# Optimization experiments

Hardware: AMD Instinct MI355X
Metric: run time of the kernel (lower is better)

The kernel has to match this reference:

```python
import jax, jax.numpy as jnp
import numpy as np

GAM1 = 1.0
GAM2 = 1.0
EPS = 0.01


def setup_inputs() -> dict:
    key = jax.random.key(0)
    kx, ky = jax.random.split(key)
    m, p, k = 16384, 512, 10
    X = jax.random.normal(kx, (m, p), dtype=jnp.float32)
    Y = jax.random.randint(ky, (m,), 0, k, dtype=jnp.int64)
    return {"X": X, "Y": Y, "num_classes": k}


def reference(X, Y, num_classes):
    # W: [p, m] (features x samples), as in the torch module (W = X.T)
    W = X.reshape(X.shape[0], -1).T
    p, m = W.shape
    I = jnp.eye(p, dtype=W.dtype)

    # ---- empirical discriminative loss ----
    scalar = p / (m * EPS)
    G = W @ W.T  # [p, p]
    discrimn = jnp.linalg.slogdet(I + GAM1 * scalar * G)[1] / 2.0

    # ---- empirical compressive loss ----
    # Pi[j] is diagonal with the one-hot membership of class j, so
    # W @ Pi[j] @ W.T == (W * mask_j) @ W.T. Build all k masked Grams at once.
    M = jax.nn.one_hot(Y, num_classes, dtype=W.dtype)  # [m, k]
    trPi = M.sum(axis=0) + 1e-8                         # [k] class counts
    # Gk[j] = sum_{i in class j} w_i w_i^T  -> [k, p, p]
    Gk = jnp.einsum('pm,mk,qm->kpq', W, M, W)
    scal = (p / (trPi * EPS))[:, None, None]
    logdets = jnp.linalg.slogdet(I[None] + scal * Gk)[1]  # [k]
    compress = jnp.sum(logdets * trPi / m) / 2.0

    return (discrimn, compress)
```

## Files before the change

kernel.cpp:

```cpp
#include <hip/hip_runtime.h>
#include <math.h>

#define P 512
#define KC 10
#define NB 32
#define EPSV 0.01f
#define TR_ROWS 448
#define XT 17024

typedef __attribute__((ext_vector_type(8))) __bf16 bf16x8;
typedef __attribute__((ext_vector_type(4))) float floatx4;

__global__ __launch_bounds__(256) void sort_k(const int* __restrict__ Y, int* __restrict__ colmap,
                                              int* __restrict__ counts, int* __restrict__ off_pad, int m){
  __shared__ int cnt[KC], offp[KC + 1], cur[KC];
  int tid = threadIdx.x;
  if (tid < KC) cnt[tid] = 0;
  __syncthreads();
  for (int i = tid; i < m; i += 256){
    int y = Y[i];
    if (y >= 0 && y < KC) atomicAdd(&cnt[y], 1);
  }
  __syncthreads();
  if (tid == 0){
    int s = 0;
    for (int j = 0; j < KC; ++j){ offp[j] = s; s += ((cnt[j] + 63) >> 6) << 6; }
    offp[KC] = s;
  }
  __syncthreads();
  if (tid < KC){ cur[tid] = offp[tid]; counts[tid] = cnt[tid]; off_pad[tid] = offp[tid]; }
  if (tid == KC) off_pad[KC] = offp[KC];
  for (int i = tid; i < XT; i += 256) colmap[i] = -1;
  __syncthreads();
  for (int i = tid; i < m; i += 256){
    int y = Y[i];
    if (y >= 0 && y < KC){
      int pos = atomicAdd(&cur[y], 1);
      colmap[pos] = i;
    }
  }
}

__global__ __launch_bounds__(256) void xt_k(const float* __restrict__ X, const int* __restrict__ colmap,
                                            __bf16* __restrict__ Xhi, __bf16* __restrict__ Xlo){
  __shared__ float T[64][65];
  int c0 = blockIdx.x * 64;
  int f0 = blockIdx.y * 64;
  int tid = threadIdx.x;

  int j = tid >> 2;
  int piece = tid & 3;
  int s = colmap[c0 + j];
  if (s >= 0){
    const float* src = X + (long)s * P + f0 + piece * 16;
    #pragma unroll
    for (int q = 0; q < 4; ++q){
      float4 v = *(const float4*)(src + q * 4);
      T[piece * 16 + q * 4 + 0][j] = v.x;
      T[piece * 16 + q * 4 + 1][j] = v.y;
      T[piece * 16 + q * 4 + 2][j] = v.z;
      T[piece * 16 + q * 4 + 3][j] = v.w;
    }
  } else {
    #pragma unroll
    for (int q = 0; q < 16; ++q) T[piece * 16 + q][j] = 0.f;
  }
  __syncthreads();

  int f = tid >> 2;
  int cp = (tid & 3) * 16;
  bf16x8 vh0, vl0, vh1, vl1;
  #pragma unroll
  for (int q = 0; q < 8; ++q){
    float x0 = T[f][cp + q];
    float x1 = T[f][cp + 8 + q];
    __bf16 h0 = (__bf16)x0, h1 = (__bf16)x1;
    vh0[q] = h0; vl0[q] = (__bf16)(x0 - (float)h0);
    vh1[q] = h1; vl1[q] = (__bf16)(x1 - (float)h1);
  }
  long base = (long)(f0 + f) * XT + c0 + cp;
  *(bf16x8*)&Xhi[base]     = vh0;
  *(bf16x8*)&Xhi[base + 8] = vh1;
  *(bf16x8*)&Xlo[base]     = vl0;
  *(bf16x8*)&Xlo[base + 8] = vl1;
}

__global__ __launch_bounds__(256) void gram_mfma(const __bf16* __restrict__ Xhi,
                                                 const __bf16* __restrict__ Xlo,
                                                 const int* __restrict__ counts,
                                                 const int* __restrict__ off_pad,
                                                 float* __restrict__ Gk){
  int cls = blockIdx.y;
  int ta = 0, rem = blockIdx.x;
  while (rem >= ta + 1){ rem -= ta + 1; ++ta; }
  int tb = rem;
  int a0 = ta * 64, b0 = tb * 64;

  int tid  = threadIdx.x;
  int lane = tid & 63;
  int wv   = tid >> 6;
  int wrow = wv >> 1, wcol = wv & 1;
  int fr   = lane & 15;
  int quad = lane >> 4;

  int cs0     = off_pad[cls];
  int nchunks = (counts[cls] + 31) >> 5;

  long arow0 = (long)(a0 + wrow * 32 + fr) * XT;
  long brow0 = (long)(b0 + wcol * 32 + fr) * XT;

  floatx4 acc[2][2];
  #pragma unroll
  for (int i = 0; i < 2; ++i)
    #pragma unroll
    for (int j = 0; j < 2; ++j) acc[i][j] = (floatx4){0.f, 0.f, 0.f, 0.f};

  for (int ch = 0; ch < nchunks; ++ch){
    long co = cs0 + ch * 32 + quad * 8;
    bf16x8 ah[2], al[2], bh[2], bl[2];
    #pragma unroll
    for (int r = 0; r < 2; ++r){
      ah[r] = *(const bf16x8*)&Xhi[arow0 + (long)r * 16 * XT + co];
      al[r] = *(const bf16x8*)&Xlo[arow0 + (long)r * 16 * XT + co];
      bh[r] = *(const bf16x8*)&Xhi[brow0 + (long)r * 16 * XT + co];
      bl[r] = *(const bf16x8*)&Xlo[brow0 + (long)r * 16 * XT + co];
    }
    #pragma unroll
    for (int ri = 0; ri < 2; ++ri)
      #pragma unroll
      for (int rj = 0; rj < 2; ++rj){
        acc[ri][rj] = __builtin_amdgcn_mfma_f32_16x16x32_bf16(al[ri], bh[rj], acc[ri][rj], 0, 0, 0);
        acc[ri][rj] = __builtin_amdgcn_mfma_f32_16x16x32_bf16(ah[ri], bl[rj], acc[ri][rj], 0, 0, 0);
        acc[ri][rj] = __builtin_amdgcn_mfma_f32_16x16x32_bf16(ah[ri], bh[rj], acc[ri][rj], 0, 0, 0);
      }
  }

  float* C = Gk + (long)cls * P * P;
  #pragma unroll
  for (int ri = 0; ri < 2; ++ri){
    int a = a0 + wrow * 32 + ri * 16 + (lane >> 4) * 4;
    #pragma unroll
    for (int rj = 0; rj < 2; ++rj){
      int b = b0 + wcol * 32 + rj * 16 + (lane & 15);
      #pragma unroll
      for (int r = 0; r < 4; ++r)
        C[(long)(a + r) * P + b] = acc[ri][rj][r];
    }
  }
}

__global__ __launch_bounds__(256) void sum10_k(float* __restrict__ Gk){
  long i = (long)blockIdx.x * 256 + threadIdx.x;
  float4 s = {0.f, 0.f, 0.f, 0.f};
  #pragma unroll
  for (int j = 0; j < KC; ++j){
    float4 v = ((const float4*)(Gk + (long)j * P * P))[i];
    s.x += v.x; s.y += v.y; s.z += v.z; s.w += v.w;
  }
  ((float4*)(Gk + (long)KC * P * P))[i] = s;
}

__global__ __launch_bounds__(512, 2) void chol_mfma(float* __restrict__ Gk,
                                                    const int* __restrict__ counts,
                                                    float* __restrict__ logdets,
                                                    float m_tot){
  __shared__ __bf16 Lhi[TR_ROWS * 32];
  __shared__ __bf16 Llo[TR_ROWS * 32];
  __shared__ float  Ld[NB * 33];
  __shared__ float  Ldr[NB];

  int mat  = blockIdx.x;
  int tid  = threadIdx.x;
  int lane = tid & 63;
  int wv   = tid >> 6;
  float* A = Gk + (long)mat * P * P;
  float sc = (mat < KC) ? ((float)P / (((float)counts[mat] + 1e-8f) * EPSV))
                        : ((float)P / (m_tot * EPSV));
  float logsum = 0.f;

  for (int s = 0; s < 16; ++s){
    int j0 = s * NB;
    int qt = P - j0 - NB;

    if (wv == 0){
      float a[NB];
      if (lane < NB){
        const float* src = A + (long)(j0 + lane) * P + j0;
        #pragma unroll
        for (int u = 0; u < NB; u += 4){
          float4 v = *(const float4*)(src + u);
          a[u] = v.x; a[u+1] = v.y; a[u+2] = v.z; a[u+3] = v.w;
        }
        if (s == 0){
          #pragma unroll
          for (int u = 0; u < NB; ++u) a[u] *= sc;
          a[lane] += 1.0f;
        }
      } else {
        #pragma unroll
        for (int u = 0; u < NB; ++u) a[u] = 0.f;
      }
      #pragma unroll
      for (int jj = 0; jj < NB; ++jj){
        float d = __shfl(a[jj], jj);
        logsum += __log2f(d);
        float inv = 1.0f / d;
        float rs  = rsqrtf(d);
        float w   = a[jj] * inv;
        #pragma unroll
        for (int l = 0; l < NB; ++l){
          if (l > jj){
            float prl = __shfl(a[l], jj);
            a[l] -= w * prl;
          }
        }
        a[jj] *= rs;
      }
      if (lane < NB){
        #pragma unroll
        for (int u = 0; u < NB; ++u) Ld[lane * 33 + u] = a[u];
        Ldr[lane] = 1.0f / a[lane];
      }
    }
    __syncthreads();

    if (qt > 0){
      if (tid < qt){
        float b[NB];
        const float* src = A + (long)(j0 + NB + tid) * P + j0;
        #pragma unroll
        for (int u = 0; u < NB; u += 4){
          float4 v = *(const float4*)(src + u);
          b[u] = v.x; b[u+1] = v.y; b[u+2] = v.z; b[u+3] = v.w;
        }
        if (s == 0){
          #pragma unroll
          for (int u = 0; u < NB; ++u) b[u] *= sc;
        }
        #pragma unroll
        for (int jj = 0; jj < NB; ++jj){
          float acc = b[jj];
          for (int u = 0; u < jj; ++u) acc -= b[u] * Ld[jj * 33 + u];
          b[jj] = acc * Ldr[jj];
        }
        int t = tid;
        #pragma unroll
        for (int c = 0; c < 4; ++c){
          int sw = (t * 4 + (c ^ ((t >> 1) & 3))) * 8;
          bf16x8 vh, vl;
          #pragma unroll
          for (int j = 0; j < 8; ++j){
            float f = b[c * 8 + j];
            __bf16 h = (__bf16)f;
            vh[j] = h;
            vl[j] = (__bf16)(f - (float)h);
          }
          *(bf16x8*)&Lhi[sw] = vh;
          *(bf16x8*)&Llo[sw] = vl;
        }
      }
    }
    __syncthreads();

    if (qt > 0){
      int tt = qt >> 5;
      int T  = tt * (tt + 1) / 2;
      int trail0 = j0 + NB;
      for (int idx = wv; idx < T; idx += 8){
        int ti = 0, rem = idx;
        while (rem >= ti + 1){ rem -= ti + 1; ++ti; }
        int tj = rem;
        int I0 = ti * 32, J0 = tj * 32;
        int c  = lane >> 4;

        bf16x8 ahi[2], alo[2], bhi[2], blo[2];
        #pragma unroll
        for (int h = 0; h < 2; ++h){
          int r1 = I0 + h * 16 + (lane & 15);
          int sw1 = (r1 * 4 + (c ^ ((r1 >> 1) & 3))) * 8;
          ahi[h] = *(const bf16x8*)&Lhi[sw1];
          alo[h] = *(const bf16x8*)&Llo[sw1];
          int r2 = J0 + h * 16 + (lane & 15);
          int sw2 = (r2 * 4 + (c ^ ((r2 >> 1) & 3))) * 8;
          bhi[h] = *(const bf16x8*)&Lhi[sw2];
          blo[h] = *(const bf16x8*)&Llo[sw2];
        }

        #pragma unroll
        for (int hi_ = 0; hi_ < 2; ++hi_){
          #pragma unroll
          for (int hj = 0; hj < 2; ++hj){
            floatx4 acc = {0.f, 0.f, 0.f, 0.f};
            acc = __builtin_amdgcn_mfma_f32_16x16x32_bf16(alo[hi_], bhi[hj], acc, 0, 0, 0);
            acc = __builtin_amdgcn_mfma_f32_16x16x32_bf16(ahi[hi_], blo[hj], acc, 0, 0, 0);
            acc = __builtin_amdgcn_mfma_f32_16x16x32_bf16(ahi[hi_], bhi[hj], acc, 0, 0, 0);
            int grow0 = trail0 + I0 + hi_ * 16 + (lane >> 4) * 4;
            int gcol  = trail0 + J0 + hj  * 16 + (lane & 15);
            #pragma unroll
            for (int r = 0; r < 4; ++r){
              long off = (long)(grow0 + r) * P + gcol;
              float v = A[off];
              if (s == 0) v = sc * v + ((grow0 + r) == gcol ? 1.f : 0.f);
              A[off] = v - acc[r];
            }
          }
        }
      }
    }
    __syncthreads();
  }

  if (tid == 0) logdets[mat] = logsum * 0.6931471805599453f;
}

__global__ __launch_bounds__(64) void final_k(const float* __restrict__ logdets,
                                              const int* __restrict__ counts,
                                              float* __restrict__ out, float m_tot){
  if (threadIdx.x == 0 && blockIdx.x == 0){
    out[0] = 0.5f * logdets[KC];
    float comp = 0.f;
    for (int j = 0; j < KC; ++j){
      float trPi = (float)counts[j] + 1e-8f;
      comp += logdets[j] * trPi / m_tot;
    }
    out[1] = 0.5f * comp;
  }
}

extern "C" void kernel_launch(void* const* d_in, const int* in_sizes, int n_in,
                              void* d_out, int out_size, void* d_ws, size_t ws_size,
                              hipStream_t stream) {
  (void)n_in; (void)out_size; (void)ws_size;
  const float* X = (const float*)d_in[0];
  const int*   Y = (const int*)d_in[1];
  int m = in_sizes[0] / P;

  float*  Gk      = (float*)d_ws;
  __bf16* Xhi     = (__bf16*)(Gk + 11L * P * P);
  __bf16* Xlo     = Xhi + (long)P * XT;
  int*    colmap  = (int*)(Xlo + (long)P * XT);
  int*    counts  = colmap + XT;
  int*    off_pad = counts + 16;
  float*  logdets = (float*)(off_pad + 17);

  sort_k<<<1, 256, 0, stream>>>(Y, colmap, counts, off_pad, m);

  dim3 xg(XT / 64, 8);
  xt_k<<<xg, 256, 0, stream>>>(X, colmap, Xhi, Xlo);

  dim3 gg(36, KC);
  gram_mfma<<<gg, 256, 0, stream>>>(Xhi, Xlo, counts, off_pad, Gk);

  sum10_k<<<P * P / 1024, 256, 0, stream>>>(Gk);

  chol_mfma<<<KC + 1, 512, 0, stream>>>(Gk, counts, logdets, (float)m);

  final_k<<<1, 64, 0, stream>>>(logdets, counts, (float*)d_out, (float)m);
}
```

Measured before the change: 457.4 us.

## Replace panel triangular solve with explicit L^-1 and split-bf16 MFMA multiply

The diagonal-block wave now explicitly inverts the 32x32 Cholesky factor via readlane-based forward substitution and stores it as hi/lo bf16 in shared memory. The panel TRSM, previously a serial per-thread 32x32 triangular solve run by only qt threads, becomes a 3-pass split-bf16 MFMA product of each 16-row tile with L^-1, spread over all waves. Shuffles in the factorization are replaced with readlane. This moves serial scalar work onto matrix cores and raises parallelism in the panel step. In exchange it adds an explicit inversion and the accuracy risk of bf16-split arithmetic with an inverted factor.

```diff
diff --git a/kernel.cpp b/kernel.cpp
--- a/kernel.cpp
+++ b/kernel.cpp
@@ -7,9 +7,14 @@
 #define EPSV 0.01f
 #define TR_ROWS 448
 #define XT 17024
+#define MSTRIDE 40
 
 typedef __attribute__((ext_vector_type(8))) __bf16 bf16x8;
 typedef __attribute__((ext_vector_type(4))) float floatx4;
+
+__device__ __forceinline__ float rdl(float x, int l){
+  return __builtin_bit_cast(float, __builtin_amdgcn_readlane(__builtin_bit_cast(int, x), l));
+}
 
 __global__ __launch_bounds__(256) void sort_k(const int* __restrict__ Y, int* __restrict__ colmap,
                                               int* __restrict__ counts, int* __restrict__ off_pad, int m){
@@ -164,10 +169,10 @@
                                                     const int* __restrict__ counts,
                                                     float* __restrict__ logdets,
                                                     float m_tot){
-  __shared__ __bf16 Lhi[TR_ROWS * 32];
-  __shared__ __bf16 Llo[TR_ROWS * 32];
-  __shared__ float  Ld[NB * 33];
-  __shared__ float  Ldr[NB];
+  __shared__ __align__(16) __bf16 Lhi[TR_ROWS * 32];
+  __shared__ __align__(16) __bf16 Llo[TR_ROWS * 32];
+  __shared__ __align__(16) __bf16 Mhi[NB * MSTRIDE];
+  __shared__ __align__(16) __bf16 Mlo[NB * MSTRIDE];
 
   int mat  = blockIdx.x;
   int tid  = threadIdx.x;
@@ -184,6 +189,7 @@
 
     if (wv == 0){
       float a[NB];
+      float dri[NB];
       if (lane < NB){
         const float* src = A + (long)(j0 + lane) * P + j0;
         #pragma unroll
@@ -202,61 +208,84 @@
       }
       #pragma unroll
       for (int jj = 0; jj < NB; ++jj){
-        float d = __shfl(a[jj], jj);
+        float d = rdl(a[jj], jj);
         logsum += __log2f(d);
         float inv = 1.0f / d;
         float rs  = rsqrtf(d);
-        float w   = a[jj] * inv;
-        #pragma unroll
-        for (int l = 0; l < NB; ++l){
-          if (l > jj){
-            float prl = __shfl(a[l], jj);
-            a[l] -= w * prl;
-          }
+        dri[jj] = rs;
+        float w = a[jj] * inv;
+        #pragma unroll
+        for (int l = jj + 1; l < NB; ++l){
+          float prl = rdl(a[l], jj);
+          a[l] = fmaf(-w, prl, a[l]);
         }
         a[jj] *= rs;
       }
+      float mcol[NB];
+      #pragma unroll
+      for (int u = 0; u < NB; ++u) mcol[u] = 0.f;
+      #pragma unroll
+      for (int r = 0; r < NB; ++r){
+        float ssum = (lane == r) ? 1.0f : 0.0f;
+        #pragma unroll
+        for (int u = 0; u < r; ++u){
+          float lru = rdl(a[u], r);
+          ssum = fmaf(-lru, mcol[u], ssum);
+        }
+        mcol[r] = ssum * dri[r];
+      }
       if (lane < NB){
         #pragma unroll
-        for (int u = 0; u < NB; ++u) Ld[lane * 33 + u] = a[u];
-        Ldr[lane] = 1.0f / a[lane];
+        for (int u = 0; u < NB; ++u){
+          float f = mcol[u];
+          __bf16 h = (__bf16)f;
+          Mhi[u * MSTRIDE + lane] = h;
+          Mlo[u * MSTRIDE + lane] = (__bf16)(f - (float)h);
+        }
       }
     }
     __syncthreads();
 
     if (qt > 0){
-      if (tid < qt){
-        float b[NB];
-        const float* src = A + (long)(j0 + NB + tid) * P + j0;
-        #pragma unroll
-        for (int u = 0; u < NB; u += 4){
-          float4 v = *(const float4*)(src + u);
-          b[u] = v.x; b[u+1] = v.y; b[u+2] = v.z; b[u+3] = v.w;
-        }
+      int ntiles = qt >> 4;
+      int r16 = lane & 15;
+      int kq  = lane >> 4;
+      for (int rt = wv; rt < ntiles; rt += 8){
+        int row = j0 + NB + rt * 16 + r16;
+        const float* src = A + (long)row * P + j0 + kq * 8;
+        float4 v0 = *(const float4*)(src);
+        float4 v1 = *(const float4*)(src + 4);
+        float f[8] = {v0.x, v0.y, v0.z, v0.w, v1.x, v1.y, v1.z, v1.w};
         if (s == 0){
           #pragma unroll
-          for (int u = 0; u < NB; ++u) b[u] *= sc;
-        }
-        #pragma unroll
-        for (int jj = 0; jj < NB; ++jj){
-          float acc = b[jj];
-          for (int u = 0; u < jj; ++u) acc -= b[u] * Ld[jj * 33 + u];
-          b[jj] = acc * Ldr[jj];
-        }
-        int t = tid;
-        #pragma unroll
-        for (int c = 0; c < 4; ++c){
-          int sw = (t * 4 + (c ^ ((t >> 1) & 3))) * 8;
-          bf16x8 vh, vl;
+          for (int u = 0; u < 8; ++u) f[u] *= sc;
+        }
+        bf16x8 ahi, alo;
+        #pragma unroll
+        for (int u = 0; u < 8; ++u){
+          __bf16 h = (__bf16)f[u];
+          ahi[u] = h;
+          alo[u] = (__bf16)(f[u] - (float)h);
+        }
+        #pragma unroll
+        for (int ng = 0; ng < 2; ++ng){
+          int mrow = ng * 16 + r16;
+          bf16x8 bhi = *(const bf16x8*)&Mhi[mrow * MSTRIDE + kq * 8];
+          bf16x8 blo = *(const bf16x8*)&Mlo[mrow * MSTRIDE + kq * 8];
+          floatx4 acc = {0.f, 0.f, 0.f, 0.f};
+          acc = __builtin_amdgcn_mfma_f32_16x16x32_bf16(alo, bhi, acc, 0, 0, 0);
+          acc = __builtin_amdgcn_mfma_f32_16x16x32_bf16(ahi, blo, acc, 0, 0, 0);
+          acc = __builtin_amdgcn_mfma_f32_16x16x32_bf16(ahi, bhi, acc, 0, 0, 0);
           #pragma unroll
-          for (int j = 0; j < 8; ++j){
-            float f = b[c * 8 + j];
-            __bf16 h = (__bf16)f;
-            vh[j] = h;
-            vl[j] = (__bf16)(f - (float)h);
+          for (int r = 0; r < 4; ++r){
+            int t  = rt * 16 + kq * 4 + r;
+            int cc = ng * 16 + r16;
+            int e  = (t * 4 + ((cc >> 3) ^ ((t >> 1) & 3))) * 8 + (cc & 7);
+            float fv = acc[r];
+            __bf16 h = (__bf16)fv;
+            Lhi[e] = h;
+            Llo[e] = (__bf16)(fv - (float)h);
           }
-          *(bf16x8*)&Lhi[sw] = vh;
-          *(bf16x8*)&Llo[sw] = vl;
         }
       }
     }
@@ -273,17 +302,17 @@
         int I0 = ti * 32, J0 = tj * 32;
         int c  = lane >> 4;
 
-        bf16x8 ahi[2], alo[2], bhi[2], blo[2];
+        bf16x8 ahi2[2], alo2[2], bhi2[2], blo2[2];
         #pragma unroll
         for (int h = 0; h < 2; ++h){
           int r1 = I0 + h * 16 + (lane & 15);
           int sw1 = (r1 * 4 + (c ^ ((r1 >> 1) & 3))) * 8;
-          ahi[h] = *(const bf16x8*)&Lhi[sw1];
-          alo[h] = *(const bf16x8*)&Llo[sw1];
+          ahi2[h] = *(const bf16x8*)&Lhi[sw1];
+          alo2[h] = *(const bf16x8*)&Llo[sw1];
           int r2 = J0 + h * 16 + (lane & 15);
           int sw2 = (r2 * 4 + (c ^ ((r2 >> 1) & 3))) * 8;
-          bhi[h] = *(const bf16x8*)&Lhi[sw2];
-          blo[h] = *(const bf16x8*)&Llo[sw2];
+          bhi2[h] = *(const bf16x8*)&Lhi[sw2];
+          blo2[h] = *(const bf16x8*)&Llo[sw2];
         }
 
         #pragma unroll
@@ -291,9 +320,9 @@
           #pragma unroll
           for (int hj = 0; hj < 2; ++hj){
             floatx4 acc = {0.f, 0.f, 0.f, 0.f};
-            acc = __builtin_amdgcn_mfma_f32_16x16x32_bf16(alo[hi_], bhi[hj], acc, 0, 0, 0);
-            acc = __builtin_amdgcn_mfma_f32_16x16x32_bf16(ahi[hi_], blo[hj], acc, 0, 0, 0);
-            acc = __builtin_amdgcn_mfma_f32_16x16x32_bf16(ahi[hi_], bhi[hj], acc, 0, 0, 0);
+            acc = __builtin_amdgcn_mfma_f32_16x16x32_bf16(alo2[hi_], bhi2[hj], acc, 0, 0, 0);
+            acc = __builtin_amdgcn_mfma_f32_16x16x32_bf16(ahi2[hi_], blo2[hj], acc, 0, 0, 0);
+            acc = __builtin_amdgcn_mfma_f32_16x16x32_bf16(ahi2[hi_], bhi2[hj], acc, 0, 0, 0);
             int grow0 = trail0 + I0 + hi_ * 16 + (lane >> 4) * 4;
             int gcol  = trail0 + J0 + hj  * 16 + (lane & 15);
             #pragma unroll
```

Measured after the change: 503.3 us. 1.1x slower.

## Split-K the class Gram kernel with atomic accumulation and register prefetch

Applied to the files above, without the earlier changes.

Splits each class's sample-chunk reduction across four blocks along a new grid z dimension. Partial tiles are accumulated into Gk with atomicAdd after a memset zeroes the buffer. This raises the grid from 360 to 1440 blocks to fill more CUs. The inner loop also double-buffers the global loads so the next chunk is fetched while the current MFMAs run. The cost is atomic traffic, an extra memset, and non-deterministic float summation order.

```diff
diff --git a/kernel.cpp b/kernel.cpp
--- a/kernel.cpp
+++ b/kernel.cpp
@@ -7,6 +7,7 @@
 #define EPSV 0.01f
 #define TR_ROWS 448
 #define XT 17024
+#define KSPLIT 4
 
 typedef __attribute__((ext_vector_type(8))) __bf16 bf16x8;
 typedef __attribute__((ext_vector_type(4))) float floatx4;
@@ -105,6 +106,9 @@
 
   int cs0     = off_pad[cls];
   int nchunks = (counts[cls] + 31) >> 5;
+  int nper    = (nchunks + KSPLIT - 1) / KSPLIT;
+  int ch0     = blockIdx.z * nper;
+  int ch1     = min(nchunks, ch0 + nper);
 
   long arow0 = (long)(a0 + wrow * 32 + fr) * XT;
   long brow0 = (long)(b0 + wcol * 32 + fr) * XT;
@@ -115,25 +119,35 @@
     #pragma unroll
     for (int j = 0; j < 2; ++j) acc[i][j] = (floatx4){0.f, 0.f, 0.f, 0.f};
 
-  for (int ch = 0; ch < nchunks; ++ch){
-    long co = cs0 + ch * 32 + quad * 8;
+#define GLOAD(AH, AL, BH, BL, CH)                                            \
+  { long co = cs0 + (long)(CH) * 32 + quad * 8;                              \
+    for (int r = 0; r < 2; ++r){                                             \
+      AH[r] = *(const bf16x8*)&Xhi[arow0 + (long)r * 16 * XT + co];          \
+      AL[r] = *(const bf16x8*)&Xlo[arow0 + (long)r * 16 * XT + co];          \
+      BH[r] = *(const bf16x8*)&Xhi[brow0 + (long)r * 16 * XT + co];          \
+      BL[r] = *(const bf16x8*)&Xlo[brow0 + (long)r * 16 * XT + co]; } }
+
+  if (ch0 < ch1){
     bf16x8 ah[2], al[2], bh[2], bl[2];
-    #pragma unroll
-    for (int r = 0; r < 2; ++r){
-      ah[r] = *(const bf16x8*)&Xhi[arow0 + (long)r * 16 * XT + co];
-      al[r] = *(const bf16x8*)&Xlo[arow0 + (long)r * 16 * XT + co];
-      bh[r] = *(const bf16x8*)&Xhi[brow0 + (long)r * 16 * XT + co];
-      bl[r] = *(const bf16x8*)&Xlo[brow0 + (long)r * 16 * XT + co];
-    }
-    #pragma unroll
-    for (int ri = 0; ri < 2; ++ri)
+    GLOAD(ah, al, bh, bl, ch0)
+    for (int ch = ch0; ch < ch1; ++ch){
+      bf16x8 nh[2], nl[2], mh[2], ml[2];
+      if (ch + 1 < ch1) GLOAD(nh, nl, mh, ml, ch + 1)
       #pragma unroll
-      for (int rj = 0; rj < 2; ++rj){
-        acc[ri][rj] = __builtin_amdgcn_mfma_f32_16x16x32_bf16(al[ri], bh[rj], acc[ri][rj], 0, 0, 0);
-        acc[ri][rj] = __builtin_amdgcn_mfma_f32_16x16x32_bf16(ah[ri], bl[rj], acc[ri][rj], 0, 0, 0);
-        acc[ri][rj] = __builtin_amdgcn_mfma_f32_16x16x32_bf16(ah[ri], bh[rj], acc[ri][rj], 0, 0, 0);
-      }
-  }
+      for (int ri = 0; ri < 2; ++ri)
+        #pragma unroll
+        for (int rj = 0; rj < 2; ++rj){
+          acc[ri][rj] = __builtin_amdgcn_mfma_f32_16x16x32_bf16(al[ri], bh[rj], acc[ri][rj], 0, 0, 0);
+          acc[ri][rj] = __builtin_amdgcn_mfma_f32_16x16x32_bf16(ah[ri], bl[rj], acc[ri][rj], 0, 0, 0);
+          acc[ri][rj] = __builtin_amdgcn_mfma_f32_16x16x32_bf16(ah[ri], bh[rj], acc[ri][rj], 0, 0, 0);
+        }
+      if (ch + 1 < ch1){
+        #pragma unroll
+        for (int r = 0; r < 2; ++r){ ah[r] = nh[r]; al[r] = nl[r]; bh[r] = mh[r]; bl[r] = ml[r]; }
+      }
+    }
+  }
+#undef GLOAD
 
   float* C = Gk + (long)cls * P * P;
   #pragma unroll
@@ -144,7 +158,7 @@
       int b = b0 + wcol * 32 + rj * 16 + (lane & 15);
       #pragma unroll
       for (int r = 0; r < 4; ++r)
-        C[(long)(a + r) * P + b] = acc[ri][rj][r];
+        atomicAdd(&C[(long)(a + r) * P + b], acc[ri][rj][r]);
     }
   }
 }
@@ -348,7 +362,9 @@
   dim3 xg(XT / 64, 8);
   xt_k<<<xg, 256, 0, stream>>>(X, colmap, Xhi, Xlo);
 
-  dim3 gg(36, KC);
+  hipMemsetAsync(Gk, 0, (size_t)KC * P * P * sizeof(float), stream);
+
+  dim3 gg(36, KC, KSPLIT);
   gram_mfma<<<gg, 256, 0, stream>>>(Xhi, Xlo, counts, off_pad, Gk);
 
   sum10_k<<<P * P / 1024, 256, 0, stream>>>(Gk);
```

Result: faster. 429.4 us (-6.1%).
